# Optimization experiments

Hardware: AMD Instinct MI355X
Metric: run time of the kernel (lower is better)

Reference implementation:

```python
import jax, jax.numpy as jnp
import numpy as np

DIM = 4096
K = 16  # 2**bits, bits=4
SCALE = 1.0 / DIM ** 0.5
# Lloyd-Max optimal 16-level quantizer centroids for N(0,1)
LLOYD_MAX_4BIT = np.array([
    -2.7326, -2.0690, -1.6181, -1.2562, -0.9424, -0.6568, -0.3881, -0.1284,
     0.1284,  0.3881,  0.6568,  0.9424,  1.2562,  1.6181,  2.0690,  2.7326,
], dtype=np.float32)


def setup_inputs() -> dict:
    key = jax.random.key(0)
    k_x, k_q = jax.random.split(key)
    x = jax.random.normal(k_x, (2048, DIM), dtype=jnp.float32)
    # Random orthogonal rotation via QR, matching torch.linalg.qr(randn(dim, dim))
    g = jax.random.normal(k_q, (DIM, DIM), dtype=jnp.float32)
    rotation, _ = jnp.linalg.qr(g)
    codebook = jnp.asarray(LLOYD_MAX_4BIT)
    return {"x": x, "rotation": rotation, "codebook": codebook}


def reference(x, rotation, codebook):
    # x: (N, dim); rotation: (dim, dim) orthogonal; codebook: (K,)
    shape = x.shape
    x_flat = x.reshape(-1, DIM).astype(jnp.float32)
    y = x_flat @ rotation.T                      # (N, dim) rotate
    y_norm = y / SCALE                           # coords ~ N(0, 1)
    # (N, dim, K) distance tensor -> argmin over codebook axis
    dists = jnp.abs(y_norm[..., None] - codebook)
    idx = jnp.argmin(dists, axis=-1)             # (N, dim) int32
    y_hat = codebook[idx] * SCALE                # gather + rescale
    x_hat = y_hat @ rotation                     # inverse rotation
    return x_hat.reshape(shape)
```

## Files before the change

### kernel.cpp

```cpp
#include <hip/hip_runtime.h>
#include <hip/hip_bf16.h>


typedef __attribute__((ext_vector_type(8))) _Float16 f16x8;
typedef __attribute__((ext_vector_type(4))) float f32x4;

__device__ __forceinline__ unsigned short f2h(float f) {
    _Float16 h = (_Float16)f;
    return *reinterpret_cast<unsigned short*>(&h);
}

__global__ __launch_bounds__(256) void convert_x_kernel(
    const float* __restrict__ x, unsigned short* __restrict__ xb) {
    const int i = (blockIdx.x * 256 + threadIdx.x) * 4;
    float4 v = *reinterpret_cast<const float4*>(x + i);
    ushort4 b;
    b.x = f2h(v.x); b.y = f2h(v.y); b.z = f2h(v.z); b.w = f2h(v.w);
    *reinterpret_cast<ushort4*>(xb + i) = b;
}

__global__ __launch_bounds__(256) void conv_rot_kernel(
    const float* __restrict__ R, unsigned short* __restrict__ Rb,
    unsigned short* __restrict__ Rt) {
    __shared__ float t[64][65];
    const int tid = threadIdx.x;
    const int tr = blockIdx.y * 64, tc = blockIdx.x * 64;
    const int r0 = tid >> 4;
    const int c4 = (tid & 15) << 2;
#pragma unroll
    for (int i = 0; i < 4; i++) {
        const int r = r0 + i * 16;
        float4 v = *reinterpret_cast<const float4*>(
            &R[(size_t)(tr + r) * 4096 + tc + c4]);
        ushort4 b;
        b.x = f2h(v.x); b.y = f2h(v.y); b.z = f2h(v.z); b.w = f2h(v.w);
        *reinterpret_cast<ushort4*>(&Rb[(size_t)(tr + r) * 4096 + tc + c4]) = b;
        t[r][c4 + 0] = v.x; t[r][c4 + 1] = v.y;
        t[r][c4 + 2] = v.z; t[r][c4 + 3] = v.w;
    }
    __syncthreads();
#pragma unroll
    for (int i = 0; i < 16; i++) {
        const int idx = tid + 256 * i;
        const int rr = idx >> 6;
        const int cc = idx & 63;
        Rt[(size_t)(tc + rr) * 4096 + tr + cc] = f2h(t[cc][rr]);
    }
}

constexpr int GK = 4096;
constexpr int BM = 128, BN = 256, BK = 32;
constexpr int NT = GK / BK;
constexpr int A_LDS = BM * BK * 2;
constexpr int BUF = (BM + BN) * BK * 2;
constexpr int LDS_DYN = 3 * BUF;

template <bool QUANT>
__global__ __launch_bounds__(512, 4) void gemm_nt_kernel(
    const unsigned short* __restrict__ A, const unsigned short* __restrict__ Bt,
    void* __restrict__ Cout, const float* __restrict__ cb16) {
    extern __shared__ char smem[];
    const int tid = threadIdx.x;
    const int lane = tid & 63;
    const int w = tid >> 6;
    const int wm = w >> 2;
    const int wn = w & 3;

    const int bid = blockIdx.x;
    const int wgid = (bid & 7) * 32 + (bid >> 3);
    const int tn = wgid & 15;
    const int tm = wgid >> 4;

    f32x4 acc[4][4];
#pragma unroll
    for (int m = 0; m < 4; m++)
#pragma unroll
        for (int n = 0; n < 4; n++) acc[m][n] = (f32x4){0.f, 0.f, 0.f, 0.f};

    const int srow = tid >> 2;
    const int scol = (((tid & 3) ^ ((srow >> 1) & 3)) << 3);
    const unsigned short* ApS = A + (size_t)(tm * BM + srow) * GK + scol;
    const unsigned short* BpS0 = Bt + (size_t)(tn * BN + srow) * GK + scol;
    const unsigned short* BpS1 = BpS0 + (size_t)128 * GK;
    const int wbase = (w << 10);

#define STAGE(dstbase)                                                         \
    {                                                                          \
        __builtin_amdgcn_global_load_lds(                                      \
            (const __attribute__((address_space(1))) void*)ApS,                \
            (__attribute__((address_space(3))) void*)(smem + (dstbase) + wbase), 16, 0, 0); \
        __builtin_amdgcn_global_load_lds(                                      \
            (const __attribute__((address_space(1))) void*)BpS0,               \
            (__attribute__((address_space(3))) void*)(smem + (dstbase) + A_LDS + wbase), 16, 0, 0); \
        __builtin_amdgcn_global_load_lds(                                      \
            (const __attribute__((address_space(1))) void*)BpS1,               \
            (__attribute__((address_space(3))) void*)(smem + (dstbase) + A_LDS + 8192 + wbase), 16, 0, 0); \
        ApS += BK; BpS0 += BK; BpS1 += BK;                                     \
    }

    const int sw = (((lane >> 4) ^ (((lane & 15) >> 1) & 3)) << 4);
    const int arow = (wm * 64 + (lane & 15)) * 64;
    const int brow = A_LDS + (wn * 64 + (lane & 15)) * 64;

#define LDA(m) (*reinterpret_cast<const f16x8*>(smem + lb + arow + (m) * 1024 + sw))
#define LDB(n) (*reinterpret_cast<const f16x8*>(smem + lb + brow + (n) * 1024 + sw))
#define MFMA_ROW(aR, r)                                                          \
    acc[r][0] = __builtin_amdgcn_mfma_f32_16x16x32_f16(aR, b0, acc[r][0], 0, 0, 0); \
    acc[r][1] = __builtin_amdgcn_mfma_f32_16x16x32_f16(aR, b1, acc[r][1], 0, 0, 0); \
    acc[r][2] = __builtin_amdgcn_mfma_f32_16x16x32_f16(aR, b2, acc[r][2], 0, 0, 0); \
    acc[r][3] = __builtin_amdgcn_mfma_f32_16x16x32_f16(aR, b3, acc[r][3], 0, 0, 0);

    STAGE(0)
    STAGE(BUF)
    asm volatile("s_waitcnt vmcnt(3)" ::: "memory");
    __builtin_amdgcn_s_barrier();
    __builtin_amdgcn_sched_barrier(0);

    int lb = 0;
    int wb = 2 * BUF;
    for (int t = 0; t < NT; ++t) {
        f16x8 a0, a1, a2, a3, b0, b1, b2, b3;
        a0 = LDA(0); a1 = LDA(1); a2 = LDA(2); a3 = LDA(3);
        b0 = LDB(0); b1 = LDB(1); b2 = LDB(2); b3 = LDB(3);
        if (t + 2 < NT) STAGE(wb)
        asm volatile("s_waitcnt lgkmcnt(0)" ::: "memory");
        __builtin_amdgcn_sched_barrier(0);
        __builtin_amdgcn_s_setprio(1);
        MFMA_ROW(a0, 0) MFMA_ROW(a1, 1) MFMA_ROW(a2, 2) MFMA_ROW(a3, 3)
        __builtin_amdgcn_s_setprio(0);
        if (t + 1 < NT) {
            if (t + 2 < NT) {
                asm volatile("s_waitcnt vmcnt(3)" ::: "memory");
            } else {
                asm volatile("s_waitcnt vmcnt(0)" ::: "memory");
            }
            __builtin_amdgcn_s_barrier();
            __builtin_amdgcn_sched_barrier(0);
            lb = (lb == 2 * BUF) ? 0 : lb + BUF;
            wb = (wb == 2 * BUF) ? 0 : wb + BUF;
        }
    }
#undef LDA
#undef LDB
#undef MFMA_ROW
#undef STAGE

    const int crow0 = tm * BM + wm * 64 + ((lane >> 4) << 2);
    const int ccol0 = tn * BN + wn * 64 + (lane & 15);
    if constexpr (QUANT) {
        float c[16];
#pragma unroll
        for (int i = 0; i < 16; i++) c[i] = cb16[i];
        unsigned short* O = (unsigned short*)Cout;
#pragma unroll
        for (int m = 0; m < 4; m++)
#pragma unroll
            for (int n = 0; n < 4; n++)
#pragma unroll
                for (int j = 0; j < 4; j++) {
                    const float yn = acc[m][n][j] * 64.0f;
                    float v = c[0];
#pragma unroll
                    for (int i = 0; i < 15; i++) {
                        const float bnd = 0.5f * (c[i] + c[i + 1]);
                        v = (yn > bnd) ? c[i + 1] : v;
                    }
                    O[(size_t)(crow0 + m * 16 + j) * 4096 + ccol0 + n * 16] =
                        f2h(v * 0.015625f);
                }
    } else {
        float* O = (float*)Cout;
#pragma unroll
        for (int m = 0; m < 4; m++)
#pragma unroll
            for (int n = 0; n < 4; n++)
#pragma unroll
                for (int j = 0; j < 4; j++)
                    O[(size_t)(crow0 + m * 16 + j) * 4096 + ccol0 + n * 16] =
                        acc[m][n][j];
    }
}

extern "C" void kernel_launch(void* const* d_in, const int* in_sizes, int n_in,
                              void* d_out, int out_size, void* d_ws,
                              size_t ws_size, hipStream_t stream) {
    const float* x = (const float*)d_in[0];
    const float* rot = (const float*)d_in[1];
    const float* cb = (const float*)d_in[2];
    float* out = (float*)d_out;

    unsigned short* Xh = (unsigned short*)d_ws;
    unsigned short* Rh = Xh + (size_t)2048 * 4096;
    unsigned short* Rt = Rh + (size_t)4096 * 4096;
    unsigned short* Yh = Rt + (size_t)4096 * 4096;

    (void)hipFuncSetAttribute(
        reinterpret_cast<const void*>(&gemm_nt_kernel<true>),
        hipFuncAttributeMaxDynamicSharedMemorySize, LDS_DYN);
    (void)hipFuncSetAttribute(
        reinterpret_cast<const void*>(&gemm_nt_kernel<false>),
        hipFuncAttributeMaxDynamicSharedMemorySize, LDS_DYN);

    convert_x_kernel<<<8192, 256, 0, stream>>>(x, Xh);
    conv_rot_kernel<<<dim3(64, 64), 256, 0, stream>>>(rot, Rh, Rt);
    gemm_nt_kernel<true><<<256, 512, LDS_DYN, stream>>>(Xh, Rh, (void*)Yh, cb);
    gemm_nt_kernel<false><<<256, 512, LDS_DYN, stream>>>(Yh, Rt, (void*)out, nullptr);
}
```

Baseline: 176.4 us.

## Deepen GEMM pipeline to four LDS stages with register double-buffered fragments

Moves the GEMM main loop from three to four LDS buffers, so global loads are issued three tiles ahead, and double-buffers the A/B register fragments so LDS reads for tile t+1 overlap the MFMAs of tile t. The loop is unrolled by two to alternate the fragment register sets. The launch bound drops to 2 waves per SIMD and LDS use grows to 96KB per block, which lowers occupancy and raises register pressure. The aim is to hide LDS and global latency better.

```diff
diff --git a/kernel.cpp b/kernel.cpp
--- a/kernel.cpp
+++ b/kernel.cpp
@@ -53,10 +53,10 @@
 constexpr int NT = GK / BK;
 constexpr int A_LDS = BM * BK * 2;
 constexpr int BUF = (BM + BN) * BK * 2;
-constexpr int LDS_DYN = 3 * BUF;
+constexpr int LDS_DYN = 4 * BUF;
 
 template <bool QUANT>
-__global__ __launch_bounds__(512, 4) void gemm_nt_kernel(
+__global__ __launch_bounds__(512, 2) void gemm_nt_kernel(
     const unsigned short* __restrict__ A, const unsigned short* __restrict__ Bt,
     void* __restrict__ Cout, const float* __restrict__ cb16) {
     extern __shared__ char smem[];
@@ -102,47 +102,72 @@
     const int arow = (wm * 64 + (lane & 15)) * 64;
     const int brow = A_LDS + (wn * 64 + (lane & 15)) * 64;
 
-#define LDA(m) (*reinterpret_cast<const f16x8*>(smem + lb + arow + (m) * 1024 + sw))
-#define LDB(n) (*reinterpret_cast<const f16x8*>(smem + lb + brow + (n) * 1024 + sw))
-#define MFMA_ROW(aR, r)                                                          \
-    acc[r][0] = __builtin_amdgcn_mfma_f32_16x16x32_f16(aR, b0, acc[r][0], 0, 0, 0); \
-    acc[r][1] = __builtin_amdgcn_mfma_f32_16x16x32_f16(aR, b1, acc[r][1], 0, 0, 0); \
-    acc[r][2] = __builtin_amdgcn_mfma_f32_16x16x32_f16(aR, b2, acc[r][2], 0, 0, 0); \
-    acc[r][3] = __builtin_amdgcn_mfma_f32_16x16x32_f16(aR, b3, acc[r][3], 0, 0, 0);
-
-    STAGE(0)
-    STAGE(BUF)
+#define LDA(rb, m) (*reinterpret_cast<const f16x8*>(smem + (rb) + arow + (m) * 1024 + sw))
+#define LDB(rb, n) (*reinterpret_cast<const f16x8*>(smem + (rb) + brow + (n) * 1024 + sw))
+#define MFMA_ALL(P)                                                               \
+    acc[0][0] = __builtin_amdgcn_mfma_f32_16x16x32_f16(P##a0, P##b0, acc[0][0], 0, 0, 0); \
+    acc[0][1] = __builtin_amdgcn_mfma_f32_16x16x32_f16(P##a0, P##b1, acc[0][1], 0, 0, 0); \
+    acc[0][2] = __builtin_amdgcn_mfma_f32_16x16x32_f16(P##a0, P##b2, acc[0][2], 0, 0, 0); \
+    acc[0][3] = __builtin_amdgcn_mfma_f32_16x16x32_f16(P##a0, P##b3, acc[0][3], 0, 0, 0); \
+    acc[1][0] = __builtin_amdgcn_mfma_f32_16x16x32_f16(P##a1, P##b0, acc[1][0], 0, 0, 0); \
+    acc[1][1] = __builtin_amdgcn_mfma_f32_16x16x32_f16(P##a1, P##b1, acc[1][1], 0, 0, 0); \
+    acc[1][2] = __builtin_amdgcn_mfma_f32_16x16x32_f16(P##a1, P##b2, acc[1][2], 0, 0, 0); \
+    acc[1][3] = __builtin_amdgcn_mfma_f32_16x16x32_f16(P##a1, P##b3, acc[1][3], 0, 0, 0); \
+    acc[2][0] = __builtin_amdgcn_mfma_f32_16x16x32_f16(P##a2, P##b0, acc[2][0], 0, 0, 0); \
+    acc[2][1] = __builtin_amdgcn_mfma_f32_16x16x32_f16(P##a2, P##b1, acc[2][1], 0, 0, 0); \
+    acc[2][2] = __builtin_amdgcn_mfma_f32_16x16x32_f16(P##a2, P##b2, acc[2][2], 0, 0, 0); \
+    acc[2][3] = __builtin_amdgcn_mfma_f32_16x16x32_f16(P##a2, P##b3, acc[2][3], 0, 0, 0); \
+    acc[3][0] = __builtin_amdgcn_mfma_f32_16x16x32_f16(P##a3, P##b0, acc[3][0], 0, 0, 0); \
+    acc[3][1] = __builtin_amdgcn_mfma_f32_16x16x32_f16(P##a3, P##b1, acc[3][1], 0, 0, 0); \
+    acc[3][2] = __builtin_amdgcn_mfma_f32_16x16x32_f16(P##a3, P##b2, acc[3][2], 0, 0, 0); \
+    acc[3][3] = __builtin_amdgcn_mfma_f32_16x16x32_f16(P##a3, P##b3, acc[3][3], 0, 0, 0);
+
+    f16x8 Xa0, Xa1, Xa2, Xa3, Xb0, Xb1, Xb2, Xb3;
+    f16x8 Ya0, Ya1, Ya2, Ya3, Yb0, Yb1, Yb2, Yb3;
+
+#define LOAD_FRAGS(P, rb)                                                      \
+    P##a0 = LDA(rb, 0); P##a1 = LDA(rb, 1); P##a2 = LDA(rb, 2); P##a3 = LDA(rb, 3); \
+    P##b0 = LDB(rb, 0); P##b1 = LDB(rb, 1); P##b2 = LDB(rb, 2); P##b3 = LDB(rb, 3);
+
+#define BODY(CUR, NXT, t)                                                      \
+    {                                                                          \
+        if ((t) + 1 < NT) { LOAD_FRAGS(NXT, (((t) + 1) & 3) * BUF) }           \
+        if ((t) + 3 < NT) STAGE((((t) + 3) & 3) * BUF)                         \
+        if ((t) + 1 < NT) {                                                    \
+            asm volatile("s_waitcnt lgkmcnt(8)" ::: "memory");                 \
+        } else {                                                               \
+            asm volatile("s_waitcnt lgkmcnt(0)" ::: "memory");                 \
+        }                                                                      \
+        __builtin_amdgcn_sched_barrier(0);                                     \
+        __builtin_amdgcn_s_setprio(1);                                         \
+        MFMA_ALL(CUR)                                                          \
+        __builtin_amdgcn_s_setprio(0);                                         \
+        if ((t) + 3 < NT) {                                                    \
+            asm volatile("s_waitcnt vmcnt(3)" ::: "memory");                   \
+        } else {                                                               \
+            asm volatile("s_waitcnt vmcnt(0)" ::: "memory");                   \
+        }                                                                      \
+        __builtin_amdgcn_s_barrier();                                          \
+        __builtin_amdgcn_sched_barrier(0);                                     \
+    }
+
+    STAGE(0 * BUF)
+    STAGE(1 * BUF)
+    STAGE(2 * BUF)
     asm volatile("s_waitcnt vmcnt(3)" ::: "memory");
     __builtin_amdgcn_s_barrier();
     __builtin_amdgcn_sched_barrier(0);
-
-    int lb = 0;
-    int wb = 2 * BUF;
-    for (int t = 0; t < NT; ++t) {
-        f16x8 a0, a1, a2, a3, b0, b1, b2, b3;
-        a0 = LDA(0); a1 = LDA(1); a2 = LDA(2); a3 = LDA(3);
-        b0 = LDB(0); b1 = LDB(1); b2 = LDB(2); b3 = LDB(3);
-        if (t + 2 < NT) STAGE(wb)
-        asm volatile("s_waitcnt lgkmcnt(0)" ::: "memory");
-        __builtin_amdgcn_sched_barrier(0);
-        __builtin_amdgcn_s_setprio(1);
-        MFMA_ROW(a0, 0) MFMA_ROW(a1, 1) MFMA_ROW(a2, 2) MFMA_ROW(a3, 3)
-        __builtin_amdgcn_s_setprio(0);
-        if (t + 1 < NT) {
-            if (t + 2 < NT) {
-                asm volatile("s_waitcnt vmcnt(3)" ::: "memory");
-            } else {
-                asm volatile("s_waitcnt vmcnt(0)" ::: "memory");
-            }
-            __builtin_amdgcn_s_barrier();
-            __builtin_amdgcn_sched_barrier(0);
-            lb = (lb == 2 * BUF) ? 0 : lb + BUF;
-            wb = (wb == 2 * BUF) ? 0 : wb + BUF;
-        }
-    }
+    LOAD_FRAGS(X, 0)
+
+    for (int t = 0; t < NT; t += 2) {
+        BODY(X, Y, t)
+        BODY(Y, X, t + 1)
+    }
+#undef BODY
+#undef LOAD_FRAGS
 #undef LDA
 #undef LDB
-#undef MFMA_ROW
+#undef MFMA_ALL
 #undef STAGE
 
     const int crow0 = tm * BM + wm * 64 + ((lane >> 4) << 2);
```

After: 180.2 us. 2.2% more time.

## Split-K both GEMMs into two halves with merge kernels for better CU occupancy

Applied to the files above, without the earlier changes.

Each GEMM is split along K into two halves, giving 512 workgroups instead of 256 so more of the MI355X's compute units are busy. Partial sums go to the output buffer and a separate fp32 slab. Separate elementwise kernels then sum the halves, quantizing for the first GEMM and plain adding for the second. This costs extra fp32 traffic (two 32MB partials written and read per GEMM) and two more launches, and is used only when the workspace is large enough.

```diff
diff --git a/kernel.cpp b/kernel.cpp
--- a/kernel.cpp
+++ b/kernel.cpp
@@ -8,6 +8,16 @@
 __device__ __forceinline__ unsigned short f2h(float f) {
     _Float16 h = (_Float16)f;
     return *reinterpret_cast<unsigned short*>(&h);
+}
+
+__device__ __forceinline__ float quant16(float yn, const float* c) {
+    float v = c[0];
+#pragma unroll
+    for (int i = 0; i < 15; i++) {
+        const float bnd = 0.5f * (c[i] + c[i + 1]);
+        v = (yn > bnd) ? c[i + 1] : v;
+    }
+    return v;
 }
 
 __global__ __launch_bounds__(256) void convert_x_kernel(
@@ -50,15 +60,15 @@
 
 constexpr int GK = 4096;
 constexpr int BM = 128, BN = 256, BK = 32;
-constexpr int NT = GK / BK;
 constexpr int A_LDS = BM * BK * 2;
 constexpr int BUF = (BM + BN) * BK * 2;
 constexpr int LDS_DYN = 3 * BUF;
 
-template <bool QUANT>
+template <int MODE, int NTK>
 __global__ __launch_bounds__(512, 4) void gemm_nt_kernel(
     const unsigned short* __restrict__ A, const unsigned short* __restrict__ Bt,
-    void* __restrict__ Cout, const float* __restrict__ cb16) {
+    void* __restrict__ Out0, float* __restrict__ Slab1,
+    const float* __restrict__ cb16) {
     extern __shared__ char smem[];
     const int tid = threadIdx.x;
     const int lane = tid & 63;
@@ -67,9 +77,18 @@
     const int wn = w & 3;
 
     const int bid = blockIdx.x;
-    const int wgid = (bid & 7) * 32 + (bid >> 3);
-    const int tn = wgid & 15;
-    const int tm = wgid >> 4;
+    const int nwg = gridDim.x;
+    const int wgid = (bid & 7) * (nwg >> 3) + (bid >> 3);
+    int tile, kb;
+    if constexpr (MODE == 2) {
+        tile = wgid >> 1;
+        kb = (wgid & 1) * (GK / 2);
+    } else {
+        tile = wgid;
+        kb = 0;
+    }
+    const int tn = tile & 15;
+    const int tm = tile >> 4;
 
     f32x4 acc[4][4];
 #pragma unroll
@@ -79,8 +98,8 @@
 
     const int srow = tid >> 2;
     const int scol = (((tid & 3) ^ ((srow >> 1) & 3)) << 3);
-    const unsigned short* ApS = A + (size_t)(tm * BM + srow) * GK + scol;
-    const unsigned short* BpS0 = Bt + (size_t)(tn * BN + srow) * GK + scol;
+    const unsigned short* ApS = A + (size_t)(tm * BM + srow) * GK + kb + scol;
+    const unsigned short* BpS0 = Bt + (size_t)(tn * BN + srow) * GK + kb + scol;
     const unsigned short* BpS1 = BpS0 + (size_t)128 * GK;
     const int wbase = (w << 10);
 
@@ -118,18 +137,18 @@
 
     int lb = 0;
     int wb = 2 * BUF;
-    for (int t = 0; t < NT; ++t) {
+    for (int t = 0; t < NTK; ++t) {
         f16x8 a0, a1, a2, a3, b0, b1, b2, b3;
         a0 = LDA(0); a1 = LDA(1); a2 = LDA(2); a3 = LDA(3);
         b0 = LDB(0); b1 = LDB(1); b2 = LDB(2); b3 = LDB(3);
-        if (t + 2 < NT) STAGE(wb)
+        if (t + 2 < NTK) STAGE(wb)
         asm volatile("s_waitcnt lgkmcnt(0)" ::: "memory");
         __builtin_amdgcn_sched_barrier(0);
         __builtin_amdgcn_s_setprio(1);
         MFMA_ROW(a0, 0) MFMA_ROW(a1, 1) MFMA_ROW(a2, 2) MFMA_ROW(a3, 3)
         __builtin_amdgcn_s_setprio(0);
-        if (t + 1 < NT) {
-            if (t + 2 < NT) {
+        if (t + 1 < NTK) {
+            if (t + 2 < NTK) {
                 asm volatile("s_waitcnt vmcnt(3)" ::: "memory");
             } else {
                 asm volatile("s_waitcnt vmcnt(0)" ::: "memory");
@@ -147,29 +166,21 @@
 
     const int crow0 = tm * BM + wm * 64 + ((lane >> 4) << 2);
     const int ccol0 = tn * BN + wn * 64 + (lane & 15);
-    if constexpr (QUANT) {
+    if constexpr (MODE == 0) {
         float c[16];
 #pragma unroll
         for (int i = 0; i < 16; i++) c[i] = cb16[i];
-        unsigned short* O = (unsigned short*)Cout;
+        unsigned short* O = (unsigned short*)Out0;
 #pragma unroll
         for (int m = 0; m < 4; m++)
 #pragma unroll
             for (int n = 0; n < 4; n++)
 #pragma unroll
-                for (int j = 0; j < 4; j++) {
-                    const float yn = acc[m][n][j] * 64.0f;
-                    float v = c[0];
-#pragma unroll
-                    for (int i = 0; i < 15; i++) {
-                        const float bnd = 0.5f * (c[i] + c[i + 1]);
-                        v = (yn > bnd) ? c[i + 1] : v;
-                    }
+                for (int j = 0; j < 4; j++)
                     O[(size_t)(crow0 + m * 16 + j) * 4096 + ccol0 + n * 16] =
-                        f2h(v * 0.015625f);
-                }
-    } else {
-        float* O = (float*)Cout;
+                        f2h(quant16(acc[m][n][j] * 64.0f, c) * 0.015625f);
+    } else if constexpr (MODE == 1) {
+        float* O = (float*)Out0;
 #pragma unroll
         for (int m = 0; m < 4; m++)
 #pragma unroll
@@ -178,7 +189,43 @@
                 for (int j = 0; j < 4; j++)
                     O[(size_t)(crow0 + m * 16 + j) * 4096 + ccol0 + n * 16] =
                         acc[m][n][j];
-    }
+    } else {
+        float* P = (wgid & 1) ? Slab1 : (float*)Out0;
+#pragma unroll
+        for (int m = 0; m < 4; m++)
+#pragma unroll
+            for (int n = 0; n < 4; n++)
+#pragma unroll
+                for (int j = 0; j < 4; j++)
+                    P[(size_t)(crow0 + m * 16 + j) * 4096 + ccol0 + n * 16] =
+                        acc[m][n][j];
+    }
+}
+
+__global__ __launch_bounds__(256) void merge_quant_kernel(
+    const float* __restrict__ p0, const float* __restrict__ p1,
+    unsigned short* __restrict__ yh, const float* __restrict__ cb16) {
+    float c[16];
+#pragma unroll
+    for (int i = 0; i < 16; i++) c[i] = cb16[i];
+    const int i = (blockIdx.x * 256 + threadIdx.x) * 4;
+    float4 a = *reinterpret_cast<const float4*>(p0 + i);
+    float4 b = *reinterpret_cast<const float4*>(p1 + i);
+    ushort4 o;
+    o.x = f2h(quant16((a.x + b.x) * 64.0f, c) * 0.015625f);
+    o.y = f2h(quant16((a.y + b.y) * 64.0f, c) * 0.015625f);
+    o.z = f2h(quant16((a.z + b.z) * 64.0f, c) * 0.015625f);
+    o.w = f2h(quant16((a.w + b.w) * 64.0f, c) * 0.015625f);
+    *reinterpret_cast<ushort4*>(yh + i) = o;
+}
+
+__global__ __launch_bounds__(256) void merge_add_kernel(
+    float* __restrict__ o, const float* __restrict__ p1) {
+    const int i = (blockIdx.x * 256 + threadIdx.x) * 4;
+    float4 a = *reinterpret_cast<const float4*>(o + i);
+    float4 b = *reinterpret_cast<const float4*>(p1 + i);
+    a.x += b.x; a.y += b.y; a.z += b.z; a.w += b.w;
+    *reinterpret_cast<float4*>(o + i) = a;
 }
 
 extern "C" void kernel_launch(void* const* d_in, const int* in_sizes, int n_in,
@@ -193,16 +240,34 @@
     unsigned short* Rh = Xh + (size_t)2048 * 4096;
     unsigned short* Rt = Rh + (size_t)4096 * 4096;
     unsigned short* Yh = Rt + (size_t)4096 * 4096;
+    float* slab1 = (float*)(Yh + (size_t)2048 * 4096);
+    const size_t need = (size_t)(16 + 32 + 32 + 16 + 32) * 1024 * 1024;
+    const bool splitk = ws_size >= need;
 
     (void)hipFuncSetAttribute(
-        reinterpret_cast<const void*>(&gemm_nt_kernel<true>),
+        reinterpret_cast<const void*>(&gemm_nt_kernel<0, 128>),
         hipFuncAttributeMaxDynamicSharedMemorySize, LDS_DYN);
     (void)hipFuncSetAttribute(
-        reinterpret_cast<const void*>(&gemm_nt_kernel<false>),
+        reinterpret_cast<const void*>(&gemm_nt_kernel<1, 128>),
+        hipFuncAttributeMaxDynamicSharedMemorySize, LDS_DYN);
+    (void)hipFuncSetAttribute(
+        reinterpret_cast<const void*>(&gemm_nt_kernel<2, 64>),
         hipFuncAttributeMaxDynamicSharedMemorySize, LDS_DYN);
 
     convert_x_kernel<<<8192, 256, 0, stream>>>(x, Xh);
     conv_rot_kernel<<<dim3(64, 64), 256, 0, stream>>>(rot, Rh, Rt);
-    gemm_nt_kernel<true><<<256, 512, LDS_DYN, stream>>>(Xh, Rh, (void*)Yh, cb);
-    gemm_nt_kernel<false><<<256, 512, LDS_DYN, stream>>>(Yh, Rt, (void*)out, nullptr);
-}
+
+    if (splitk) {
+        gemm_nt_kernel<2, 64><<<512, 512, LDS_DYN, stream>>>(
+            Xh, Rh, (void*)out, slab1, cb);
+        merge_quant_kernel<<<8192, 256, 0, stream>>>(out, slab1, Yh, cb);
+        gemm_nt_kernel<2, 64><<<512, 512, LDS_DYN, stream>>>(
+            Yh, Rt, (void*)out, slab1, nullptr);
+        merge_add_kernel<<<8192, 256, 0, stream>>>(out, slab1);
+    } else {
+        gemm_nt_kernel<0, 128><<<256, 512, LDS_DYN, stream>>>(
+            Xh, Rh, (void*)Yh, nullptr, cb);
+        gemm_nt_kernel<1, 128><<<256, 512, LDS_DYN, stream>>>(
+            Yh, Rt, (void*)out, nullptr, nullptr);
+    }
+}
```

Result: slower. 232.3 us (+31.7%).

## Split K across warp pairs with BK=64 and larger per-wave output tiles

Applied to the files above, without the earlier changes.

Doubles the K tile to 64 and splits the eight waves into two K-halves, each with four waves covering a 64x128 sub-tile (4x8 MFMA accumulators). The two halves are then reduced through LDS before the quantize or store epilogue. This raises register use per wave, since launch bounds drop to 2 blocks per SM and LDS per buffer doubles. In exchange it halves the number of barrier iterations and increases fragment reuse per LDS read. It also adds an LDS reduction step, and half the waves sit idle during the epilogue.

```diff
diff --git a/kernel.cpp b/kernel.cpp
--- a/kernel.cpp
+++ b/kernel.cpp
@@ -8,6 +8,16 @@
 __device__ __forceinline__ unsigned short f2h(float f) {
     _Float16 h = (_Float16)f;
     return *reinterpret_cast<unsigned short*>(&h);
+}
+
+__device__ __forceinline__ float quant16(float yn, const float* c) {
+    float v = c[0];
+#pragma unroll
+    for (int i = 0; i < 15; i++) {
+        const float bnd = 0.5f * (c[i] + c[i + 1]);
+        v = (yn > bnd) ? c[i + 1] : v;
+    }
+    return v;
 }
 
 __global__ __launch_bounds__(256) void convert_x_kernel(
@@ -49,79 +59,91 @@
 }
 
 constexpr int GK = 4096;
-constexpr int BM = 128, BN = 256, BK = 32;
+constexpr int BM = 128, BN = 256, BK = 64;
 constexpr int NT = GK / BK;
 constexpr int A_LDS = BM * BK * 2;
 constexpr int BUF = (BM + BN) * BK * 2;
 constexpr int LDS_DYN = 3 * BUF;
 
 template <bool QUANT>
-__global__ __launch_bounds__(512, 4) void gemm_nt_kernel(
+__global__ __launch_bounds__(512, 2) void gemm_nt_kernel(
     const unsigned short* __restrict__ A, const unsigned short* __restrict__ Bt,
     void* __restrict__ Cout, const float* __restrict__ cb16) {
     extern __shared__ char smem[];
     const int tid = threadIdx.x;
     const int lane = tid & 63;
     const int w = tid >> 6;
-    const int wm = w >> 2;
-    const int wn = w & 3;
+    const int pos = w & 3;
+    const int wm = pos >> 1;
+    const int wn = pos & 1;
+    const int kp = w >> 2;
 
     const int bid = blockIdx.x;
     const int wgid = (bid & 7) * 32 + (bid >> 3);
     const int tn = wgid & 15;
     const int tm = wgid >> 4;
 
-    f32x4 acc[4][4];
+    f32x4 acc[4][8];
 #pragma unroll
     for (int m = 0; m < 4; m++)
 #pragma unroll
-        for (int n = 0; n < 4; n++) acc[m][n] = (f32x4){0.f, 0.f, 0.f, 0.f};
-
-    const int srow = tid >> 2;
-    const int scol = (((tid & 3) ^ ((srow >> 1) & 3)) << 3);
-    const unsigned short* ApS = A + (size_t)(tm * BM + srow) * GK + scol;
+        for (int n = 0; n < 8; n++) acc[m][n] = (f32x4){0.f, 0.f, 0.f, 0.f};
+
+    const int srow = tid >> 3;
+    const int scol = (((tid & 7) ^ (srow & 7)) << 3);
+    const unsigned short* ApS0 = A + (size_t)(tm * BM + srow) * GK + scol;
+    const unsigned short* ApS1 = ApS0 + (size_t)64 * GK;
     const unsigned short* BpS0 = Bt + (size_t)(tn * BN + srow) * GK + scol;
-    const unsigned short* BpS1 = BpS0 + (size_t)128 * GK;
+    const unsigned short* BpS1 = BpS0 + (size_t)64 * GK;
+    const unsigned short* BpS2 = BpS0 + (size_t)128 * GK;
+    const unsigned short* BpS3 = BpS0 + (size_t)192 * GK;
     const int wbase = (w << 10);
 
+#define GLL(src, off)                                                          \
+    __builtin_amdgcn_global_load_lds(                                          \
+        (const __attribute__((address_space(1))) void*)(src),                  \
+        (__attribute__((address_space(3))) void*)(smem + (off) + wbase), 16, 0, 0);
 #define STAGE(dstbase)                                                         \
     {                                                                          \
-        __builtin_amdgcn_global_load_lds(                                      \
-            (const __attribute__((address_space(1))) void*)ApS,                \
-            (__attribute__((address_space(3))) void*)(smem + (dstbase) + wbase), 16, 0, 0); \
-        __builtin_amdgcn_global_load_lds(                                      \
-            (const __attribute__((address_space(1))) void*)BpS0,               \
-            (__attribute__((address_space(3))) void*)(smem + (dstbase) + A_LDS + wbase), 16, 0, 0); \
-        __builtin_amdgcn_global_load_lds(                                      \
-            (const __attribute__((address_space(1))) void*)BpS1,               \
-            (__attribute__((address_space(3))) void*)(smem + (dstbase) + A_LDS + 8192 + wbase), 16, 0, 0); \
-        ApS += BK; BpS0 += BK; BpS1 += BK;                                     \
-    }
-
-    const int sw = (((lane >> 4) ^ (((lane & 15) >> 1) & 3)) << 4);
-    const int arow = (wm * 64 + (lane & 15)) * 64;
-    const int brow = A_LDS + (wn * 64 + (lane & 15)) * 64;
-
-#define LDA(m) (*reinterpret_cast<const f16x8*>(smem + lb + arow + (m) * 1024 + sw))
-#define LDB(n) (*reinterpret_cast<const f16x8*>(smem + lb + brow + (n) * 1024 + sw))
+        GLL(ApS0, (dstbase) + 0)                                               \
+        GLL(ApS1, (dstbase) + 8192)                                            \
+        GLL(BpS0, (dstbase) + 16384)                                           \
+        GLL(BpS1, (dstbase) + 24576)                                           \
+        GLL(BpS2, (dstbase) + 32768)                                           \
+        GLL(BpS3, (dstbase) + 40960)                                           \
+        ApS0 += BK; ApS1 += BK; BpS0 += BK; BpS1 += BK; BpS2 += BK; BpS3 += BK;\
+    }
+
+    const int frow = lane & 15;
+    const int sw = (((kp * 4 + (lane >> 4)) ^ (frow & 7)) << 4);
+    const int arow = (wm * 64 + frow) * 128;
+    const int brow = (wn * 128 + frow) * 128;
+
+#define LDA(m) (*reinterpret_cast<const f16x8*>(smem + lb + arow + (m) * 2048 + sw))
+#define LDB(n) (*reinterpret_cast<const f16x8*>(smem + lb + A_LDS + brow + (n) * 2048 + sw))
 #define MFMA_ROW(aR, r)                                                          \
     acc[r][0] = __builtin_amdgcn_mfma_f32_16x16x32_f16(aR, b0, acc[r][0], 0, 0, 0); \
     acc[r][1] = __builtin_amdgcn_mfma_f32_16x16x32_f16(aR, b1, acc[r][1], 0, 0, 0); \
     acc[r][2] = __builtin_amdgcn_mfma_f32_16x16x32_f16(aR, b2, acc[r][2], 0, 0, 0); \
-    acc[r][3] = __builtin_amdgcn_mfma_f32_16x16x32_f16(aR, b3, acc[r][3], 0, 0, 0);
+    acc[r][3] = __builtin_amdgcn_mfma_f32_16x16x32_f16(aR, b3, acc[r][3], 0, 0, 0); \
+    acc[r][4] = __builtin_amdgcn_mfma_f32_16x16x32_f16(aR, b4, acc[r][4], 0, 0, 0); \
+    acc[r][5] = __builtin_amdgcn_mfma_f32_16x16x32_f16(aR, b5, acc[r][5], 0, 0, 0); \
+    acc[r][6] = __builtin_amdgcn_mfma_f32_16x16x32_f16(aR, b6, acc[r][6], 0, 0, 0); \
+    acc[r][7] = __builtin_amdgcn_mfma_f32_16x16x32_f16(aR, b7, acc[r][7], 0, 0, 0);
 
     STAGE(0)
     STAGE(BUF)
-    asm volatile("s_waitcnt vmcnt(3)" ::: "memory");
+    asm volatile("s_waitcnt vmcnt(6)" ::: "memory");
     __builtin_amdgcn_s_barrier();
     __builtin_amdgcn_sched_barrier(0);
 
     int lb = 0;
     int wb = 2 * BUF;
     for (int t = 0; t < NT; ++t) {
-        f16x8 a0, a1, a2, a3, b0, b1, b2, b3;
+        f16x8 a0, a1, a2, a3, b0, b1, b2, b3, b4, b5, b6, b7;
         a0 = LDA(0); a1 = LDA(1); a2 = LDA(2); a3 = LDA(3);
         b0 = LDB(0); b1 = LDB(1); b2 = LDB(2); b3 = LDB(3);
+        b4 = LDB(4); b5 = LDB(5); b6 = LDB(6); b7 = LDB(7);
         if (t + 2 < NT) STAGE(wb)
         asm volatile("s_waitcnt lgkmcnt(0)" ::: "memory");
         __builtin_amdgcn_sched_barrier(0);
@@ -130,7 +152,7 @@
         __builtin_amdgcn_s_setprio(0);
         if (t + 1 < NT) {
             if (t + 2 < NT) {
-                asm volatile("s_waitcnt vmcnt(3)" ::: "memory");
+                asm volatile("s_waitcnt vmcnt(6)" ::: "memory");
             } else {
                 asm volatile("s_waitcnt vmcnt(0)" ::: "memory");
             }
@@ -144,9 +166,24 @@
 #undef LDB
 #undef MFMA_ROW
 #undef STAGE
-
-    const int crow0 = tm * BM + wm * 64 + ((lane >> 4) << 2);
-    const int ccol0 = tn * BN + wn * 64 + (lane & 15);
+#undef GLL
+
+    __syncthreads();
+    if (kp == 1) {
+#pragma unroll
+        for (int m = 0; m < 4; m++)
+#pragma unroll
+            for (int n = 0; n < 8; n++)
+                *reinterpret_cast<f32x4*>(
+                    smem + pos * 32768 + (m * 8 + n) * 1024 + lane * 16) =
+                    acc[m][n];
+    }
+    __syncthreads();
+    if (kp == 1) return;
+
+    const int g = lane >> 4;
+    const int crow0 = tm * BM + wm * 64 + (g << 2);
+    const int ccol0 = tn * BN + wn * 128 + frow;
     if constexpr (QUANT) {
         float c[16];
 #pragma unroll
@@ -155,29 +192,29 @@
 #pragma unroll
         for (int m = 0; m < 4; m++)
 #pragma unroll
-            for (int n = 0; n < 4; n++)
+            for (int n = 0; n < 8; n++) {
+                f32x4 other = *reinterpret_cast<const f32x4*>(
+                    smem + pos * 32768 + (m * 8 + n) * 1024 + lane * 16);
 #pragma unroll
                 for (int j = 0; j < 4; j++) {
-                    const float yn = acc[m][n][j] * 64.0f;
-                    float v = c[0];
-#pragma unroll
-                    for (int i = 0; i < 15; i++) {
-                        const float bnd = 0.5f * (c[i] + c[i + 1]);
-                        v = (yn > bnd) ? c[i + 1] : v;
-                    }
+                    const float s = acc[m][n][j] + other[j];
                     O[(size_t)(crow0 + m * 16 + j) * 4096 + ccol0 + n * 16] =
-                        f2h(v * 0.015625f);
+                        f2h(quant16(s * 64.0f, c) * 0.015625f);
                 }
+            }
     } else {
         float* O = (float*)Cout;
 #pragma unroll
         for (int m = 0; m < 4; m++)
 #pragma unroll
-            for (int n = 0; n < 4; n++)
+            for (int n = 0; n < 8; n++) {
+                f32x4 other = *reinterpret_cast<const f32x4*>(
+                    smem + pos * 32768 + (m * 8 + n) * 1024 + lane * 16);
 #pragma unroll
                 for (int j = 0; j < 4; j++)
                     O[(size_t)(crow0 + m * 16 + j) * 4096 + ccol0 + n * 16] =
-                        acc[m][n][j];
+                        acc[m][n][j] + other[j];
+            }
     }
 }
 
```

After: 164.1 us. -7.0%, faster.
